# Performance work log

Measured on AMD Instinct MI355X. Metric: run time of the kernel, lower is better.

Reference implementation:

```python
import jax, jax.numpy as jnp
import numpy as np

N, E = 25000, 400000
S, NB, RMAX, EMB, MAXA = 8, 8, 5.0, 16, 10
MULS, DIMS = (8, 4, 4), (1, 3, 5)  # irreps_output = 8x0e + 4x1o + 4x2e -> dim 40
WNUM = S * S * sum(MULS)  # 1024 generated TP weights per edge


def _silu(x):
    return x * jax.nn.sigmoid(x)


def _mlp(x, Ws, bs):
    for W, b in zip(Ws[:-1], bs[:-1]):
        x = _silu(x @ W + b)
    return x @ Ws[-1] + bs[-1]


def _sh_l012(v):
    """Real spherical harmonics l=0,1,2 on normalized v, component normalization (||Y_l||=sqrt(2l+1))."""
    n = jnp.sqrt(jnp.sum(v * v, axis=-1, keepdims=True) + 1e-12)
    u = v / n
    x, y, z = u[:, 0], u[:, 1], u[:, 2]
    s3, s5, s15 = 3.0 ** 0.5, 5.0 ** 0.5, 15.0 ** 0.5
    return jnp.stack([
        jnp.ones_like(x),                      # l=0
        s3 * x, s3 * y, s3 * z,                # l=1
        s15 * x * y, s15 * y * z,
        (s5 / 2.0) * (2.0 * z * z - x * x - y * y),
        s15 * x * z, (s15 / 2.0) * (x * x - y * y),  # l=2
    ], axis=-1)  # [E, 9]


def _radial(r):
    """Gaussian radial basis embedding with hard cutoff at RMAX (matches _radial_embedding)."""
    x = jnp.clip(r / RMAX, 0.0, 1.0)
    idx = jnp.arange(NB, dtype=r.dtype)
    centers = idx / (NB - 1)
    sigma = 1.0 / (NB - 1)
    emb = jnp.exp(-0.5 * ((x[:, None] - centers[None, :]) / sigma) ** 2)
    emb = emb * (NB ** 0.5)
    return emb * (r <= RMAX).astype(r.dtype)[:, None]  # [E, NB]


def _forward(pos, edge_shifts, cell, atom_table, fw1, fb1, fw2, fb2, fw3, fb3,
             gw1, gb1, gw2, gb2, gw3, gb3, gw4, gb4, A, batch, edge_src, edge_dst):
    # edge geometry (with periodic shifts)
    edge_cells = cell[batch[edge_src]]                          # [E,3,3]
    shift_vecs = jnp.einsum('ni,nij->nj', edge_shifts, edge_cells)
    edge_vec = pos[edge_dst] - pos[edge_src] + shift_vecs       # [E,3]
    r = jnp.sqrt(jnp.sum(edge_vec * edge_vec, axis=-1) + 1e-12)

    # node scalar features: embedding -> MLP (fitnet1)
    Ai = _mlp(atom_table[A], [fw1, fw2, fw3], [fb1, fb2, fb3])  # [N, S]

    # full tensor product of source scalars with edge SH: f[e,i,m] = Ai[src,i] * sh[e,m]
    sh = _sh_l012(edge_vec)                                     # [E, 9]
    f = Ai[edge_src][:, :, None] * sh[:, None, :]               # [E, S, 9]

    # per-edge generated weights from radial embedding
    w = _mlp(_radial(r), [gw1, gw2, gw3, gw4], [gb1, gb2, gb3, gb4])  # [E, WNUM]

    # fully connected TP with scalar second input: per output l,
    #   out[e,u,m] = alpha * sum_{i,j} w[e,i,j,u] * f_l[e,i,m] * Ai_dst[e,j],  alpha = 1/sqrt(S*S)
    Ad = Ai[edge_dst]                                           # [E, S]
    alpha = 1.0 / S
    outs, off_sh, off_w = [], 0, 0
    for mul_out, dim in zip(MULS, DIMS):
        f_l = f[:, :, off_sh:off_sh + dim]                      # [E, S, dim]
        w_l = w[:, off_w:off_w + S * S * mul_out].reshape(-1, S, S, mul_out)
        o = alpha * jnp.einsum('eim,ej,eiju->eum', f_l, Ad, w_l)  # [E, mul_out, dim]
        outs.append(o.reshape(-1, mul_out * dim))
        off_sh += dim
        off_w += S * S * mul_out
    edge_features = jnp.concatenate(outs, axis=-1)              # [E, 40]

    # scatter mean over destination nodes
    ones = jnp.ones((edge_dst.shape[0],), edge_features.dtype)
    count = jnp.maximum(jax.ops.segment_sum(ones, edge_dst, num_segments=N), 1.0)
    acc = jax.ops.segment_sum(edge_features, edge_dst, num_segments=N)
    return acc / count[:, None]                                 # [N, 40]


def setup_inputs() -> dict:
    key = jax.random.key(0)
    ks = jax.random.split(key, 20)
    def nrm(k, shape, scale=1.0):
        return (jax.random.normal(k, shape, dtype=jnp.float32) * scale).astype(jnp.float32)
    d = {}
    d['pos'] = nrm(ks[0], (N, 3), 1.5)
    d['edge_shifts'] = jnp.zeros((E, 3), jnp.float32)
    d['cell'] = nrm(ks[1], (1, 3, 3))
    d['atom_table'] = nrm(ks[2], (MAXA, EMB))
    dims_f = [EMB, 64, 32, S]
    for i in range(3):
        d[f'fw{i+1}'] = nrm(ks[3 + i], (dims_f[i], dims_f[i + 1]), 1.0 / np.sqrt(dims_f[i]))
        d[f'fb{i+1}'] = jnp.zeros((dims_f[i + 1],), jnp.float32)
    dims_g = [NB, 64, 64, 64, WNUM]
    for i in range(4):
        d[f'gw{i+1}'] = nrm(ks[6 + i], (dims_g[i], dims_g[i + 1]), 1.0 / np.sqrt(dims_g[i]))
        d[f'gb{i+1}'] = jnp.zeros((dims_g[i + 1],), jnp.float32)
    d['A'] = jax.random.randint(ks[10], (N,), 0, MAXA, dtype=jnp.int32)
    d['batch'] = jnp.zeros((N,), jnp.int32)
    d['edge_src'] = jax.random.randint(ks[11], (E,), 0, N, dtype=jnp.int32)
    d['edge_dst'] = jax.random.randint(ks[12], (E,), 0, N, dtype=jnp.int32)
    return d


def reference(pos, edge_shifts, cell, atom_table, fw1, fb1, fw2, fb2, fw3, fb3,
              gw1, gb1, gw2, gb2, gw3, gb3, gw4, gb4, A, batch, edge_src, edge_dst):
    return _forward(pos, edge_shifts, cell, atom_table, fw1, fb1, fw2, fb2, fw3, fb3,
                    gw1, gb1, gw2, gb2, gw3, gb3, gw4, gb4, A, batch, edge_src, edge_dst)
```

## Files before the change

kernel.cpp:

```cpp
#include <hip/hip_runtime.h>
#include <hip/hip_bf16.h>
#include <math.h>


typedef __attribute__((ext_vector_type(8))) short short8;
typedef __attribute__((ext_vector_type(4))) float f32x4;

#define EROW 28

__device__ __forceinline__ float silu_f(float x) {
    float e = __expf(-x);
    return x * __builtin_amdgcn_rcpf(1.0f + e);
}
__device__ __forceinline__ float silu_exact(float x) { return x / (1.0f + __expf(-x)); }

__device__ __forceinline__ unsigned short bf16r(float f) {
    union { float f; unsigned u; } v; v.f = f;
    return (unsigned short)((v.u + 0x7fffu + ((v.u >> 16) & 1u)) >> 16);
}
__device__ __forceinline__ unsigned pkcvt(float lo, float hi) {
    union { __hip_bfloat162 h; unsigned u; } v;
    v.h = __float22bfloat162_rn(float2{lo, hi});
    return v.u;
}
__device__ __forceinline__ float bflo(unsigned u) {
    union { unsigned u; float f; } v; v.u = u << 16; return v.f;
}
__device__ __forceinline__ float bfhi(unsigned u) {
    union { unsigned u; float f; } v; v.u = u & 0xffff0000u; return v.f;
}

__global__ __launch_bounds__(256) void setup_kernel(
    const float* __restrict__ gw4, const float* __restrict__ gb4,
    const float* __restrict__ gw1, const float* __restrict__ gw2,
    const float* __restrict__ gw3,
    unsigned short* __restrict__ W4pk, unsigned short* __restrict__ gw1Tp,
    unsigned short* __restrict__ gw2T, unsigned short* __restrict__ gw3T,
    unsigned short* __restrict__ gb4T2,
    const int* __restrict__ edge_dst, int* __restrict__ cnt_i,
    int* __restrict__ rank0, int n_edges)
{
    int b = blockIdx.x;
    if (b < 300) {
        int idx = b * 256 + threadIdx.x;
        if (idx < 65536) {
            int k = idx >> 10, col = idx & 1023;
            int p, u;
            if (col < 512)      { p = col >> 3;          u = col & 7; }
            else if (col < 768) { p = (col - 512) >> 2;  u = 8 + ((col - 512) & 3); }
            else                { p = (col - 768) >> 2;  u = 12 + ((col - 768) & 3); }
            W4pk[p * 1024 + u * 64 + k] = bf16r(gw4[idx]);
        } else if (idx < 67584) {
            int t = idx - 65536; int n = t >> 5, k = t & 31;
            gw1Tp[t] = (k < 8) ? bf16r(gw1[k * 64 + n]) : (unsigned short)0;
        } else if (idx < 71680) {
            int t = idx - 67584; int n = t >> 6, k = t & 63;
            gw2T[t] = bf16r(gw2[k * 64 + n]);
        } else if (idx < 75776) {
            int t = idx - 71680; int n = t >> 6, k = t & 63;
            gw3T[t] = bf16r(gw3[k * 64 + n]);
        } else if (idx < 76800) {
            int t = idx - 75776; int u = t >> 6, p = t & 63;
            int colb = (u < 8) ? (p * 8 + u)
                     : (u < 12) ? (512 + p * 4 + (u - 8))
                                : (768 + p * 4 + (u - 12));
            gb4T2[t] = bf16r(gb4[colb]);
        }
        return;
    }
    int e = (b - 300) * 256 + threadIdx.x;
    if (e < n_edges) rank0[e] = atomicAdd(&cnt_i[edge_dst[e]], 1);
}

__global__ __launch_bounds__(1024) void mid_kernel(
    const float* __restrict__ atom_table, const int* __restrict__ A,
    const float* __restrict__ fw1, const float* __restrict__ fb1,
    const float* __restrict__ fw2, const float* __restrict__ fb2,
    const float* __restrict__ fw3, const float* __restrict__ fb3,
    float* __restrict__ Ai, int n_atoms, int na_blk,
    const int* __restrict__ cnt, int* __restrict__ off)
{
    __shared__ int s[1024];
    int tid = threadIdx.x;
    int b = blockIdx.x;

    if (b < na_blk) {
        int n = b * 1024 + tid;
        if (n >= n_atoms) return;
        const float4* ap = (const float4*)(atom_table + (size_t)A[n] * 16);
        float4 a0 = ap[0], a1 = ap[1], a2 = ap[2], a3 = ap[3];
        float a[16] = {a0.x, a0.y, a0.z, a0.w, a1.x, a1.y, a1.z, a1.w,
                       a2.x, a2.y, a2.z, a2.w, a3.x, a3.y, a3.z, a3.w};

        float h2[32];
#pragma unroll
        for (int t = 0; t < 32; ++t) h2[t] = fb2[t];

#pragma unroll 4
        for (int k = 0; k < 64; ++k) {
            float h = fb1[k];
#pragma unroll
            for (int j = 0; j < 16; ++j) h += a[j] * fw1[j * 64 + k];
            h = silu_exact(h);
#pragma unroll
            for (int t = 0; t < 32; ++t) h2[t] += h * fw2[k * 32 + t];
        }

        float o[8];
#pragma unroll
        for (int t = 0; t < 8; ++t) o[t] = fb3[t];
#pragma unroll 4
        for (int k = 0; k < 32; ++k) {
            float x = silu_exact(h2[k]);
#pragma unroll
            for (int t = 0; t < 8; ++t) o[t] += x * fw3[k * 8 + t];
        }
        float* op = Ai + (size_t)n * 8;
        *(float4*)op       = float4{o[0], o[1], o[2], o[3]};
        *(float4*)(op + 4) = float4{o[4], o[5], o[6], o[7]};
        return;
    }

    int chunk = (n_atoms + 1023) / 1024;
    int start = tid * chunk;
    int end = min(start + chunk, n_atoms);
    int sum = 0;
    for (int i = start; i < end; ++i) sum += cnt[i];
    s[tid] = sum;
    __syncthreads();
    for (int d = 1; d < 1024; d <<= 1) {
        int v = (tid >= d) ? s[tid - d] : 0;
        __syncthreads();
        s[tid] += v;
        __syncthreads();
    }
    int run = (tid == 0) ? 0 : s[tid - 1];
    for (int i = start; i < end; ++i) {
        off[i] = run; run += cnt[i];
    }
    if (tid == 1023) off[n_atoms] = s[1023];
}

__global__ __launch_bounds__(64, 4) void edge_fused(
    const float* __restrict__ pos, const float* __restrict__ edge_shifts,
    const float* __restrict__ cell, const int* __restrict__ batch,
    const int* __restrict__ edge_src, const int* __restrict__ edge_dst,
    const float* __restrict__ Ai,
    const float* __restrict__ gb1, const float* __restrict__ gb2,
    const float* __restrict__ gb3,
    const unsigned short* __restrict__ gw1Tp, const unsigned short* __restrict__ gw2T,
    const unsigned short* __restrict__ gw3T,
    const unsigned short* __restrict__ W4pk, const unsigned short* __restrict__ gb4T2,
    const int* __restrict__ off, const int* __restrict__ rank0,
    float* __restrict__ erow, int n_edges)
{
    __shared__ __align__(16) char smem[8448];
    unsigned short* s_hh = (unsigned short*)smem;
    unsigned* s_c2 = (unsigned*)smem;

    int lane = threadIdx.x;
    int eb = blockIdx.x * 64;
    int quad = lane >> 4, col = lane & 15;

    int ec = min(eb + lane, n_edges - 1);
    int src = edge_src[ec], dst = edge_dst[ec];
    int rk = off[dst] + rank0[ec];

    uint4 em4;
    {
        int b = batch[src];
        const float* C = cell + b * 9;
        float es0 = edge_shifts[ec * 3 + 0];
        float es1 = edge_shifts[ec * 3 + 1];
        float es2 = edge_shifts[ec * 3 + 2];
        float vx = pos[dst * 3 + 0] - pos[src * 3 + 0] + es0 * C[0] + es1 * C[3] + es2 * C[6];
        float vy = pos[dst * 3 + 1] - pos[src * 3 + 1] + es0 * C[1] + es1 * C[4] + es2 * C[7];
        float vz = pos[dst * 3 + 2] - pos[src * 3 + 2] + es0 * C[2] + es1 * C[5] + es2 * C[8];
        float r2 = vx * vx + vy * vy + vz * vz + 1e-12f;
        float r = sqrtf(r2);
        float inv = 1.0f / r;
        float x = vx * inv, y = vy * inv, z = vz * inv;

        float xr = fminf(r * 0.2f, 1.0f);
        float cutoff = (r <= 5.0f) ? 2.8284271247461903f : 0.0f;
        float em[8];
#pragma unroll
        for (int k = 0; k < 8; ++k) {
            float d = (xr - (float)k * (1.0f / 7.0f)) * 7.0f;
            em[k] = __expf(-0.5f * d * d) * cutoff;
        }
        em4 = make_uint4(pkcvt(em[0], em[1]), pkcvt(em[2], em[3]),
                         pkcvt(em[4], em[5]), pkcvt(em[6], em[7]));

        const float s3 = 1.7320508075688772f;
        const float s5 = 2.23606797749979f;
        const float s15 = 3.872983346207417f;
        float* op = erow + (size_t)rk * EROW + 16;
        *(float4*)op = float4{1.0f, s3 * x, s3 * y, s3 * z};
        *(float4*)(op + 4) = float4{s15 * x * y, s15 * y * z,
                                    0.5f * s5 * (2.0f * z * z - x * x - y * y),
                                    s15 * x * z};
        op[8] = 0.5f * s15 * (x * x - y * y);
    }

#pragma unroll
    for (int s = 0; s < 4; ++s) {
        int sl = s * 16 + col;
        union { unsigned u[4]; short8 s8; } ua;
        ua.u[0] = (unsigned)__shfl((int)em4.x, sl, 64);
        ua.u[1] = (unsigned)__shfl((int)em4.y, sl, 64);
        ua.u[2] = (unsigned)__shfl((int)em4.z, sl, 64);
        ua.u[3] = (unsigned)__shfl((int)em4.w, sl, 64);
        short8 a = ua.s8;
        if (quad != 0) {
            short8 z = {0, 0, 0, 0, 0, 0, 0, 0};
            a = z;
        }
#pragma unroll
        for (int nt = 0; nt < 4; ++nt) {
            int n = nt * 16 + col;
            short8 b = *(const short8*)(gw1Tp + n * 32 + quad * 8);
            float bb = gb1[n];
            f32x4 d = {bb, bb, bb, bb};
            d = __builtin_amdgcn_mfma_f32_16x16x32_bf16(a, b, d, 0, 0, 0);
            unsigned u01 = pkcvt(silu_f(d[0]), silu_f(d[1]));
            unsigned u23 = pkcvt(silu_f(d[2]), silu_f(d[3]));
            unsigned short* bp2 = &s_hh[(s * 16 + quad * 4) * 66 + n];
            bp2[0]   = (unsigned short)(u01 & 0xffffu);
            bp2[66]  = (unsigned short)(u01 >> 16);
            bp2[132] = (unsigned short)(u23 & 0xffffu);
            bp2[198] = (unsigned short)(u23 >> 16);
        }
    }

#pragma unroll 1
    for (int layer = 0; layer < 2; ++layer) {
        const unsigned short* WT = layer ? gw3T : gw2T;
        const float* gb = layer ? gb3 : gb2;

        short8 a0[4], a1[4];
#pragma unroll
        for (int s = 0; s < 4; ++s) {
            a0[s] = *(const short8*)&s_hh[(s * 16 + col) * 66 + quad * 8];
            a1[s] = *(const short8*)&s_hh[(s * 16 + col) * 66 + 32 + quad * 8];
        }

#pragma unroll
        for (int nt = 0; nt < 4; ++nt) {
            int n = nt * 16 + col;
            short8 b0 = *(const short8*)(WT + n * 64 + quad * 8);
            short8 b1 = *(const short8*)(WT + n * 64 + 32 + quad * 8);
            float bb = gb[n];
#pragma unroll
            for (int s = 0; s < 4; ++s) {
                f32x4 d = {bb, bb, bb, bb};
                d = __builtin_amdgcn_mfma_f32_16x16x32_bf16(a0[s], b0, d, 0, 0, 0);
                d = __builtin_amdgcn_mfma_f32_16x16x32_bf16(a1[s], b1, d, 0, 0, 0);
                unsigned u01 = pkcvt(silu_f(d[0]), silu_f(d[1]));
                unsigned u23 = pkcvt(silu_f(d[2]), silu_f(d[3]));
                unsigned short* bp2 = &s_hh[(s * 16 + quad * 4) * 66 + n];
                bp2[0]   = (unsigned short)(u01 & 0xffffu);
                bp2[66]  = (unsigned short)(u01 >> 16);
                bp2[132] = (unsigned short)(u23 & 0xffffu);
                bp2[198] = (unsigned short)(u23 >> 16);
            }
        }
    }

    short8 aH0[4], aH1[4];
#pragma unroll
    for (int s = 0; s < 4; ++s) {
        aH0[s] = *(const short8*)&s_hh[(s * 16 + col) * 66 + quad * 8];
        aH1[s] = *(const short8*)&s_hh[(s * 16 + col) * 66 + 32 + quad * 8];
    }

    {
        const float4* asp = (const float4*)(Ai + (size_t)src * 8);
        float4 A0 = asp[0], A1 = asp[1];
        const float4* adp = (const float4*)(Ai + (size_t)dst * 8);
        float4 B0 = adp[0], B1 = adp[1];
        float as[8] = {A0.x, A0.y, A0.z, A0.w, A1.x, A1.y, A1.z, A1.w};
        float ad[8] = {B0.x, B0.y, B0.z, B0.w, B1.x, B1.y, B1.z, B1.w};
#pragma unroll
        for (int pp = 0; pp < 32; ++pp) {
            int p = pp * 2;
            float av = as[p >> 3];
            s_c2[pp * 66 + lane] = pkcvt(av * ad[p & 7], av * ad[(p & 7) + 1]);
        }
    }

    f32x4 g[4];
    {
        const unsigned short* bbp = gb4T2 + col * 64 + quad * 8;
        short8 b0 = *(const short8*)bbp;
        short8 b1 = *(const short8*)(bbp + 32);
        f32x4 zero4 = {0.0f, 0.0f, 0.0f, 0.0f};
#pragma unroll
        for (int s = 0; s < 4; ++s) {
            int ebase = s * 16 + col;
            union { unsigned u[4]; short8 s8; } ua, ub;
#pragma unroll
            for (int t = 0; t < 4; ++t) ua.u[t] = s_c2[(quad * 4 + t) * 66 + ebase];
#pragma unroll
            for (int t = 0; t < 4; ++t) ub.u[t] = s_c2[(16 + quad * 4 + t) * 66 + ebase];
            f32x4 d = __builtin_amdgcn_mfma_f32_16x16x32_bf16(ua.s8, b0, zero4, 0, 0, 0);
            g[s] = __builtin_amdgcn_mfma_f32_16x16x32_bf16(ub.s8, b1, d, 0, 0, 0);
        }
    }

    const unsigned short* wb = W4pk + col * 64 + quad * 8;
    const char* cbase = (const char*)s_c2 + quad * 16;
    f32x4 zero4 = {0.0f, 0.0f, 0.0f, 0.0f};

    short8 Pb0[2], Pb1[2], Qb0[2], Qb1[2];
    Pb0[0] = *(const short8*)(wb);
    Pb1[0] = *(const short8*)(wb + 32);
    Qb0[0] = *(const short8*)(wb + 1024);
    Qb1[0] = *(const short8*)(wb + 1056);
    Pb0[1] = *(const short8*)(wb + 2048);
    Pb1[1] = *(const short8*)(wb + 2080);
    Qb0[1] = *(const short8*)(wb + 3072);
    Qb1[1] = *(const short8*)(wb + 3104);

#pragma unroll 2
    for (int pp = 0; pp < 32; ++pp) {
        int slot = pp & 1;
        short8 b0 = Pb0[slot], b1 = Pb1[slot], e0 = Qb0[slot], e1 = Qb1[slot];
        const unsigned short* nw = wb + (2 * pp + 4) * 1024;
        Pb0[slot] = *(const short8*)(nw);
        Pb1[slot] = *(const short8*)(nw + 32);
        Qb0[slot] = *(const short8*)(nw + 1024);
        Qb1[slot] = *(const short8*)(nw + 1056);

        uint4 cc[4];
#pragma unroll
        for (int s = 0; s < 4; ++s)
            cc[s] = *(const uint4*)(cbase + pp * 264 + s * 64);

        f32x4 d[4], d2[4];
#pragma unroll
        for (int s = 0; s < 4; ++s) {
            f32x4 t = __builtin_amdgcn_mfma_f32_16x16x32_bf16(aH0[s], b0, zero4, 0, 0, 0);
            d[s] = __builtin_amdgcn_mfma_f32_16x16x32_bf16(aH1[s], b1, t, 0, 0, 0);
        }
#pragma unroll
        for (int s = 0; s < 4; ++s) {
            f32x4 t = __builtin_amdgcn_mfma_f32_16x16x32_bf16(aH0[s], e0, zero4, 0, 0, 0);
            d2[s] = __builtin_amdgcn_mfma_f32_16x16x32_bf16(aH1[s], e1, t, 0, 0, 0);
        }
#pragma unroll
        for (int s = 0; s < 4; ++s) {
            const unsigned* cu = (const unsigned*)&cc[s];
#pragma unroll
            for (int r = 0; r < 4; ++r) {
                unsigned u = cu[r];
                g[s][r] += bflo(u) * d[s][r];
                g[s][r] += bfhi(u) * d2[s][r];
            }
        }
    }

    const float alpha = 0.125f;
#pragma unroll
    for (int s = 0; s < 4; ++s) {
#pragma unroll
        for (int r = 0; r < 4; ++r) {
            int el = s * 16 + quad * 4 + r;
            int rkv = __shfl(rk, el, 64);
            if (eb + el < n_edges)
                erow[(size_t)rkv * EROW + col] = alpha * g[s][r];
        }
    }
}

__global__ __launch_bounds__(256) void gather_kernel(
    const int* __restrict__ off, const float* __restrict__ erow,
    float* __restrict__ out, int n_atoms)
{
    __shared__ float s_rows[4][8][30];
    int w = threadIdx.x >> 6, lane = threadIdx.x & 63;
    int a = blockIdx.x * 4 + w;
    if (a >= n_atoms) return;
    int beg = off[a], end = off[a + 1];

    int f = min(lane, 39);
    int u, shi;
    if (f < 8)       { u = f;                 shi = 0; }
    else if (f < 20) { u = 8 + (f - 8) / 3;   shi = 1 + (f - 8) % 3; }
    else             { u = 12 + (f - 20) / 5; shi = 4 + (f - 20) % 5; }

    int rsub = lane >> 3, csub = lane & 7;
    float val = 0.0f;
    for (int i = beg; i < end; i += 8) {
        int nr = min(8, end - i);
        int ri = i + rsub;
        if (csub < 7) {
            float4 v = (ri < end) ? *(const float4*)(erow + (size_t)ri * EROW + csub * 4)
                                  : float4{0.0f, 0.0f, 0.0f, 0.0f};
            *(float2*)&s_rows[w][rsub][csub * 4]     = float2{v.x, v.y};
            *(float2*)&s_rows[w][rsub][csub * 4 + 2] = float2{v.z, v.w};
        }
#pragma unroll
        for (int j = 0; j < 8; ++j) {
            float prod = s_rows[w][j][u] * s_rows[w][j][16 + shi];
            val += (j < nr) ? prod : 0.0f;
        }
    }
    if (lane < 40) {
        float c = (float)max(end - beg, 1);
        out[(size_t)a * 40 + lane] = val / c;
    }
}

static inline size_t align256(size_t x) { return (x + 255) & ~(size_t)255; }

extern "C" void kernel_launch(void* const* d_in, const int* in_sizes, int n_in,
                              void* d_out, int out_size, void* d_ws, size_t ws_size,
                              hipStream_t stream)
{
    const float* pos         = (const float*)d_in[0];
    const float* edge_shifts = (const float*)d_in[1];
    const float* cell        = (const float*)d_in[2];
    const float* atom_table  = (const float*)d_in[3];
    const float* fw1 = (const float*)d_in[4];
    const float* fb1 = (const float*)d_in[5];
    const float* fw2 = (const float*)d_in[6];
    const float* fb2 = (const float*)d_in[7];
    const float* fw3 = (const float*)d_in[8];
    const float* fb3 = (const float*)d_in[9];
    const float* gw1 = (const float*)d_in[10];
    const float* gb1 = (const float*)d_in[11];
    const float* gw2 = (const float*)d_in[12];
    const float* gb2 = (const float*)d_in[13];
    const float* gw3 = (const float*)d_in[14];
    const float* gb3 = (const float*)d_in[15];
    const float* gw4 = (const float*)d_in[16];
    const float* gb4 = (const float*)d_in[17];
    const int* A        = (const int*)d_in[18];
    const int* batch    = (const int*)d_in[19];
    const int* edge_src = (const int*)d_in[20];
    const int* edge_dst = (const int*)d_in[21];

    int n_atoms = in_sizes[18];
    int n_edges = in_sizes[20];

    char* w = (char*)d_ws;
    float* Ai = (float*)w;                      w += align256((size_t)n_atoms * 8 * 4);
    int* cnt_i = (int*)w;                       w += align256((size_t)n_atoms * 4);
    int* off = (int*)w;                         w += align256((size_t)(n_atoms + 1) * 4);
    int* rank0 = (int*)w;                       w += align256((size_t)n_edges * 4);
    unsigned short* W4pk = (unsigned short*)w;  w += align256((size_t)65536 * 2);
    unsigned short* gw1Tp = (unsigned short*)w; w += align256((size_t)2048 * 2);
    unsigned short* gw2T = (unsigned short*)w;  w += align256((size_t)4096 * 2);
    unsigned short* gw3T = (unsigned short*)w;  w += align256((size_t)4096 * 2);
    unsigned short* gb4T2 = (unsigned short*)w; w += align256((size_t)1024 * 2);
    float* erow = (float*)w;                    w += align256((size_t)n_edges * EROW * 4);

    float* out = (float*)d_out;

    hipMemsetAsync(cnt_i, 0, sizeof(int) * (size_t)n_atoms, stream);

    int e_blk = (n_edges + 255) / 256;
    setup_kernel<<<300 + e_blk, 256, 0, stream>>>(
        gw4, gb4, gw1, gw2, gw3, W4pk, gw1Tp, gw2T, gw3T, gb4T2,
        edge_dst, cnt_i, rank0, n_edges);

    int na_blk = (n_atoms + 1023) / 1024;
    mid_kernel<<<na_blk + 1, 1024, 0, stream>>>(
        atom_table, A, fw1, fb1, fw2, fb2, fw3, fb3,
        Ai, n_atoms, na_blk, cnt_i, off);

    edge_fused<<<(n_edges + 63) / 64, 64, 0, stream>>>(
        pos, edge_shifts, cell, batch, edge_src, edge_dst, Ai,
        gb1, gb2, gb3, gw1Tp, gw2T, gw3T, W4pk, gb4T2, off, rank0, erow, n_edges);

    gather_kernel<<<(n_atoms + 3) / 4, 256, 0, stream>>>(off, erow, out, n_atoms);
}
```

Before: 302.3 us.

## Process two 64-edge tiles per wave to reuse loaded weight fragments

Each single-wave block now handles two edge tiles, with a separate LDS buffer per tile, and shares every gw1/gw2/gw3/W4 weight fragment load across both tiles' MFMAs. This halves global/L2 weight traffic per edge in the dominant 32-iteration W4 loop and doubles independent MFMA work available for latency hiding. In exchange, register pressure roughly doubles (launch bounds relaxed from 4 to 2 waves per SIMD), LDS per block doubles, and the number of blocks is halved, which lowers occupancy and could cause spills.

```diff
diff --git a/kernel.cpp b/kernel.cpp
--- a/kernel.cpp
+++ b/kernel.cpp
@@ -141,7 +141,7 @@
     if (tid == 1023) off[n_atoms] = s[1023];
 }
 
-__global__ __launch_bounds__(64, 4) void edge_fused(
+__global__ __launch_bounds__(64, 2) void edge_fused(
     const float* __restrict__ pos, const float* __restrict__ edge_shifts,
     const float* __restrict__ cell, const int* __restrict__ batch,
     const int* __restrict__ edge_src, const int* __restrict__ edge_dst,
@@ -154,28 +154,29 @@
     const int* __restrict__ off, const int* __restrict__ rank0,
     float* __restrict__ erow, int n_edges)
 {
-    __shared__ __align__(16) char smem[8448];
-    unsigned short* s_hh = (unsigned short*)smem;
-    unsigned* s_c2 = (unsigned*)smem;
+    __shared__ __align__(16) char smem[2][8448];
 
     int lane = threadIdx.x;
-    int eb = blockIdx.x * 64;
     int quad = lane >> 4, col = lane & 15;
 
-    int ec = min(eb + lane, n_edges - 1);
-    int src = edge_src[ec], dst = edge_dst[ec];
-    int rk = off[dst] + rank0[ec];
-
-    uint4 em4;
-    {
-        int b = batch[src];
+    int src[2], dst[2], rk[2];
+    uint4 em4[2];
+
+#pragma unroll
+    for (int t = 0; t < 2; ++t) {
+        int eb = (blockIdx.x * 2 + t) * 64;
+        int ec = min(eb + lane, n_edges - 1);
+        src[t] = edge_src[ec]; dst[t] = edge_dst[ec];
+        rk[t] = off[dst[t]] + rank0[ec];
+
+        int b = batch[src[t]];
         const float* C = cell + b * 9;
         float es0 = edge_shifts[ec * 3 + 0];
         float es1 = edge_shifts[ec * 3 + 1];
         float es2 = edge_shifts[ec * 3 + 2];
-        float vx = pos[dst * 3 + 0] - pos[src * 3 + 0] + es0 * C[0] + es1 * C[3] + es2 * C[6];
-        float vy = pos[dst * 3 + 1] - pos[src * 3 + 1] + es0 * C[1] + es1 * C[4] + es2 * C[7];
-        float vz = pos[dst * 3 + 2] - pos[src * 3 + 2] + es0 * C[2] + es1 * C[5] + es2 * C[8];
+        float vx = pos[dst[t] * 3 + 0] - pos[src[t] * 3 + 0] + es0 * C[0] + es1 * C[3] + es2 * C[6];
+        float vy = pos[dst[t] * 3 + 1] - pos[src[t] * 3 + 1] + es0 * C[1] + es1 * C[4] + es2 * C[7];
+        float vz = pos[dst[t] * 3 + 2] - pos[src[t] * 3 + 2] + es0 * C[2] + es1 * C[5] + es2 * C[8];
         float r2 = vx * vx + vy * vy + vz * vz + 1e-12f;
         float r = sqrtf(r2);
         float inv = 1.0f / r;
@@ -189,13 +190,13 @@
             float d = (xr - (float)k * (1.0f / 7.0f)) * 7.0f;
             em[k] = __expf(-0.5f * d * d) * cutoff;
         }
-        em4 = make_uint4(pkcvt(em[0], em[1]), pkcvt(em[2], em[3]),
-                         pkcvt(em[4], em[5]), pkcvt(em[6], em[7]));
+        em4[t] = make_uint4(pkcvt(em[0], em[1]), pkcvt(em[2], em[3]),
+                            pkcvt(em[4], em[5]), pkcvt(em[6], em[7]));
 
         const float s3 = 1.7320508075688772f;
         const float s5 = 2.23606797749979f;
         const float s15 = 3.872983346207417f;
-        float* op = erow + (size_t)rk * EROW + 16;
+        float* op = erow + (size_t)rk[t] * EROW + 16;
         *(float4*)op = float4{1.0f, s3 * x, s3 * y, s3 * z};
         *(float4*)(op + 4) = float4{s15 * x * y, s15 * y * z,
                                     0.5f * s5 * (2.0f * z * z - x * x - y * y),
@@ -206,30 +207,38 @@
 #pragma unroll
     for (int s = 0; s < 4; ++s) {
         int sl = s * 16 + col;
-        union { unsigned u[4]; short8 s8; } ua;
-        ua.u[0] = (unsigned)__shfl((int)em4.x, sl, 64);
-        ua.u[1] = (unsigned)__shfl((int)em4.y, sl, 64);
-        ua.u[2] = (unsigned)__shfl((int)em4.z, sl, 64);
-        ua.u[3] = (unsigned)__shfl((int)em4.w, sl, 64);
-        short8 a = ua.s8;
-        if (quad != 0) {
-            short8 z = {0, 0, 0, 0, 0, 0, 0, 0};
-            a = z;
+        short8 aT[2];
+#pragma unroll
+        for (int t = 0; t < 2; ++t) {
+            union { unsigned u[4]; short8 s8; } ua;
+            ua.u[0] = (unsigned)__shfl((int)em4[t].x, sl, 64);
+            ua.u[1] = (unsigned)__shfl((int)em4[t].y, sl, 64);
+            ua.u[2] = (unsigned)__shfl((int)em4[t].z, sl, 64);
+            ua.u[3] = (unsigned)__shfl((int)em4[t].w, sl, 64);
+            short8 a = ua.s8;
+            if (quad != 0) {
+                short8 z = {0, 0, 0, 0, 0, 0, 0, 0};
+                a = z;
+            }
+            aT[t] = a;
         }
 #pragma unroll
         for (int nt = 0; nt < 4; ++nt) {
             int n = nt * 16 + col;
             short8 b = *(const short8*)(gw1Tp + n * 32 + quad * 8);
             float bb = gb1[n];
-            f32x4 d = {bb, bb, bb, bb};
-            d = __builtin_amdgcn_mfma_f32_16x16x32_bf16(a, b, d, 0, 0, 0);
-            unsigned u01 = pkcvt(silu_f(d[0]), silu_f(d[1]));
-            unsigned u23 = pkcvt(silu_f(d[2]), silu_f(d[3]));
-            unsigned short* bp2 = &s_hh[(s * 16 + quad * 4) * 66 + n];
-            bp2[0]   = (unsigned short)(u01 & 0xffffu);
-            bp2[66]  = (unsigned short)(u01 >> 16);
-            bp2[132] = (unsigned short)(u23 & 0xffffu);
-            bp2[198] = (unsigned short)(u23 >> 16);
+#pragma unroll
+            for (int t = 0; t < 2; ++t) {
+                f32x4 d = {bb, bb, bb, bb};
+                d = __builtin_amdgcn_mfma_f32_16x16x32_bf16(aT[t], b, d, 0, 0, 0);
+                unsigned u01 = pkcvt(silu_f(d[0]), silu_f(d[1]));
+                unsigned u23 = pkcvt(silu_f(d[2]), silu_f(d[3]));
+                unsigned short* bp2 = (unsigned short*)smem[t] + (s * 16 + quad * 4) * 66 + n;
+                bp2[0]   = (unsigned short)(u01 & 0xffffu);
+                bp2[66]  = (unsigned short)(u01 >> 16);
+                bp2[132] = (unsigned short)(u23 & 0xffffu);
+                bp2[198] = (unsigned short)(u23 >> 16);
+            }
         }
     }
 
@@ -238,11 +247,15 @@
         const unsigned short* WT = layer ? gw3T : gw2T;
         const float* gb = layer ? gb3 : gb2;
 
-        short8 a0[4], a1[4];
-#pragma unroll
-        for (int s = 0; s < 4; ++s) {
-            a0[s] = *(const short8*)&s_hh[(s * 16 + col) * 66 + quad * 8];
-            a1[s] = *(const short8*)&s_hh[(s * 16 + col) * 66 + 32 + quad * 8];
+        short8 a0[2][4], a1[2][4];
+#pragma unroll
+        for (int t = 0; t < 2; ++t) {
+            const unsigned short* hh = (const unsigned short*)smem[t];
+#pragma unroll
+            for (int s = 0; s < 4; ++s) {
+                a0[t][s] = *(const short8*)&hh[(s * 16 + col) * 66 + quad * 8];
+                a1[t][s] = *(const short8*)&hh[(s * 16 + col) * 66 + 32 + quad * 8];
+            }
         }
 
 #pragma unroll
@@ -252,32 +265,41 @@
             short8 b1 = *(const short8*)(WT + n * 64 + 32 + quad * 8);
             float bb = gb[n];
 #pragma unroll
-            for (int s = 0; s < 4; ++s) {
-                f32x4 d = {bb, bb, bb, bb};
-                d = __builtin_amdgcn_mfma_f32_16x16x32_bf16(a0[s], b0, d, 0, 0, 0);
-                d = __builtin_amdgcn_mfma_f32_16x16x32_bf16(a1[s], b1, d, 0, 0, 0);
-                unsigned u01 = pkcvt(silu_f(d[0]), silu_f(d[1]));
-                unsigned u23 = pkcvt(silu_f(d[2]), silu_f(d[3]));
-                unsigned short* bp2 = &s_hh[(s * 16 + quad * 4) * 66 + n];
-                bp2[0]   = (unsigned short)(u01 & 0xffffu);
-                bp2[66]  = (unsigned short)(u01 >> 16);
-                bp2[132] = (unsigned short)(u23 & 0xffffu);
-                bp2[198] = (unsigned short)(u23 >> 16);
-            }
-        }
-    }
-
-    short8 aH0[4], aH1[4];
-#pragma unroll
-    for (int s = 0; s < 4; ++s) {
-        aH0[s] = *(const short8*)&s_hh[(s * 16 + col) * 66 + quad * 8];
-        aH1[s] = *(const short8*)&s_hh[(s * 16 + col) * 66 + 32 + quad * 8];
-    }
-
-    {
-        const float4* asp = (const float4*)(Ai + (size_t)src * 8);
+            for (int t = 0; t < 2; ++t) {
+#pragma unroll
+                for (int s = 0; s < 4; ++s) {
+                    f32x4 d = {bb, bb, bb, bb};
+                    d = __builtin_amdgcn_mfma_f32_16x16x32_bf16(a0[t][s], b0, d, 0, 0, 0);
+                    d = __builtin_amdgcn_mfma_f32_16x16x32_bf16(a1[t][s], b1, d, 0, 0, 0);
+                    unsigned u01 = pkcvt(silu_f(d[0]), silu_f(d[1]));
+                    unsigned u23 = pkcvt(silu_f(d[2]), silu_f(d[3]));
+                    unsigned short* bp2 = (unsigned short*)smem[t] + (s * 16 + quad * 4) * 66 + n;
+                    bp2[0]   = (unsigned short)(u01 & 0xffffu);
+                    bp2[66]  = (unsigned short)(u01 >> 16);
+                    bp2[132] = (unsigned short)(u23 & 0xffffu);
+                    bp2[198] = (unsigned short)(u23 >> 16);
+                }
+            }
+        }
+    }
+
+    short8 aH0[2][4], aH1[2][4];
+#pragma unroll
+    for (int t = 0; t < 2; ++t) {
+        const unsigned short* hh = (const unsigned short*)smem[t];
+#pragma unroll
+        for (int s = 0; s < 4; ++s) {
+            aH0[t][s] = *(const short8*)&hh[(s * 16 + col) * 66 + quad * 8];
+            aH1[t][s] = *(const short8*)&hh[(s * 16 + col) * 66 + 32 + quad * 8];
+        }
+    }
+
+#pragma unroll
+    for (int t = 0; t < 2; ++t) {
+        unsigned* s_c2 = (unsigned*)smem[t];
+        const float4* asp = (const float4*)(Ai + (size_t)src[t] * 8);
         float4 A0 = asp[0], A1 = asp[1];
-        const float4* adp = (const float4*)(Ai + (size_t)dst * 8);
+        const float4* adp = (const float4*)(Ai + (size_t)dst[t] * 8);
         float4 B0 = adp[0], B1 = adp[1];
         float as[8] = {A0.x, A0.y, A0.z, A0.w, A1.x, A1.y, A1.z, A1.w};
         float ad[8] = {B0.x, B0.y, B0.z, B0.w, B1.x, B1.y, B1.z, B1.w};
@@ -289,27 +311,32 @@
         }
     }
 
-    f32x4 g[4];
+    f32x4 g[2][4];
     {
         const unsigned short* bbp = gb4T2 + col * 64 + quad * 8;
         short8 b0 = *(const short8*)bbp;
         short8 b1 = *(const short8*)(bbp + 32);
         f32x4 zero4 = {0.0f, 0.0f, 0.0f, 0.0f};
 #pragma unroll
-        for (int s = 0; s < 4; ++s) {
-            int ebase = s * 16 + col;
-            union { unsigned u[4]; short8 s8; } ua, ub;
-#pragma unroll
-            for (int t = 0; t < 4; ++t) ua.u[t] = s_c2[(quad * 4 + t) * 66 + ebase];
-#pragma unroll
-            for (int t = 0; t < 4; ++t) ub.u[t] = s_c2[(16 + quad * 4 + t) * 66 + ebase];
-            f32x4 d = __builtin_amdgcn_mfma_f32_16x16x32_bf16(ua.s8, b0, zero4, 0, 0, 0);
-            g[s] = __builtin_amdgcn_mfma_f32_16x16x32_bf16(ub.s8, b1, d, 0, 0, 0);
+        for (int t = 0; t < 2; ++t) {
+            const unsigned* s_c2 = (const unsigned*)smem[t];
+#pragma unroll
+            for (int s = 0; s < 4; ++s) {
+                int ebase = s * 16 + col;
+                union { unsigned u[4]; short8 s8; } ua, ub;
+#pragma unroll
+                for (int q = 0; q < 4; ++q) ua.u[q] = s_c2[(quad * 4 + q) * 66 + ebase];
+#pragma unroll
+                for (int q = 0; q < 4; ++q) ub.u[q] = s_c2[(16 + quad * 4 + q) * 66 + ebase];
+                f32x4 d = __builtin_amdgcn_mfma_f32_16x16x32_bf16(ua.s8, b0, zero4, 0, 0, 0);
+                g[t][s] = __builtin_amdgcn_mfma_f32_16x16x32_bf16(ub.s8, b1, d, 0, 0, 0);
+            }
         }
     }
 
     const unsigned short* wb = W4pk + col * 64 + quad * 8;
-    const char* cbase = (const char*)s_c2 + quad * 16;
+    const char* cb0 = (const char*)smem[0] + quad * 16;
+    const char* cb1 = (const char*)smem[1] + quad * 16;
     f32x4 zero4 = {0.0f, 0.0f, 0.0f, 0.0f};
 
     short8 Pb0[2], Pb1[2], Qb0[2], Qb1[2];
@@ -332,43 +359,40 @@
         Qb0[slot] = *(const short8*)(nw + 1024);
         Qb1[slot] = *(const short8*)(nw + 1056);
 
-        uint4 cc[4];
-#pragma unroll
-        for (int s = 0; s < 4; ++s)
-            cc[s] = *(const uint4*)(cbase + pp * 264 + s * 64);
-
-        f32x4 d[4], d2[4];
+#pragma unroll
+        for (int t = 0; t < 2; ++t) {
+            const char* cbase = t ? cb1 : cb0;
+#pragma unroll
+            for (int s = 0; s < 4; ++s) {
+                uint4 cc = *(const uint4*)(cbase + pp * 264 + s * 64);
+                f32x4 x1 = __builtin_amdgcn_mfma_f32_16x16x32_bf16(aH0[t][s], b0, zero4, 0, 0, 0);
+                f32x4 d  = __builtin_amdgcn_mfma_f32_16x16x32_bf16(aH1[t][s], b1, x1, 0, 0, 0);
+                f32x4 x2 = __builtin_amdgcn_mfma_f32_16x16x32_bf16(aH0[t][s], e0, zero4, 0, 0, 0);
+                f32x4 d2 = __builtin_amdgcn_mfma_f32_16x16x32_bf16(aH1[t][s], e1, x2, 0, 0, 0);
+                const unsigned* cu = (const unsigned*)&cc;
+#pragma unroll
+                for (int r = 0; r < 4; ++r) {
+                    unsigned u = cu[r];
+                    g[t][s][r] += bflo(u) * d[r];
+                    g[t][s][r] += bfhi(u) * d2[r];
+                }
+            }
+        }
+    }
+
+    const float alpha = 0.125f;
+#pragma unroll
+    for (int t = 0; t < 2; ++t) {
+        int eb = (blockIdx.x * 2 + t) * 64;
 #pragma unroll
         for (int s = 0; s < 4; ++s) {
-            f32x4 t = __builtin_amdgcn_mfma_f32_16x16x32_bf16(aH0[s], b0, zero4, 0, 0, 0);
-            d[s] = __builtin_amdgcn_mfma_f32_16x16x32_bf16(aH1[s], b1, t, 0, 0, 0);
-        }
-#pragma unroll
-        for (int s = 0; s < 4; ++s) {
-            f32x4 t = __builtin_amdgcn_mfma_f32_16x16x32_bf16(aH0[s], e0, zero4, 0, 0, 0);
-            d2[s] = __builtin_amdgcn_mfma_f32_16x16x32_bf16(aH1[s], e1, t, 0, 0, 0);
-        }
-#pragma unroll
-        for (int s = 0; s < 4; ++s) {
-            const unsigned* cu = (const unsigned*)&cc[s];
 #pragma unroll
             for (int r = 0; r < 4; ++r) {
-                unsigned u = cu[r];
-                g[s][r] += bflo(u) * d[s][r];
-                g[s][r] += bfhi(u) * d2[s][r];
-            }
-        }
-    }
-
-    const float alpha = 0.125f;
-#pragma unroll
-    for (int s = 0; s < 4; ++s) {
-#pragma unroll
-        for (int r = 0; r < 4; ++r) {
-            int el = s * 16 + quad * 4 + r;
-            int rkv = __shfl(rk, el, 64);
-            if (eb + el < n_edges)
-                erow[(size_t)rkv * EROW + col] = alpha * g[s][r];
+                int el = s * 16 + quad * 4 + r;
+                int rkv = __shfl(rk[t], el, 64);
+                if (eb + el < n_edges)
+                    erow[(size_t)rkv * EROW + col] = alpha * g[t][s][r];
+            }
         }
     }
 }
@@ -470,7 +494,8 @@
         atom_table, A, fw1, fb1, fw2, fb2, fw3, fb3,
         Ai, n_atoms, na_blk, cnt_i, off);
 
-    edge_fused<<<(n_edges + 63) / 64, 64, 0, stream>>>(
+    int n_tiles = (n_edges + 63) / 64;
+    edge_fused<<<(n_tiles + 1) / 2, 64, 0, stream>>>(
         pos, edge_shifts, cell, batch, edge_src, edge_dst, Ai,
         gb1, gb2, gb3, gw1Tp, gw2T, gw3T, W4pk, gb4T2, off, rank0, erow, n_edges);
 
```

After: 311.5 us. +3.0%, slower.
